# Performance work log

Hardware: AMD Instinct MI355X
Metric: run time of the kernel (lower is better)

The kernel has to match this reference:

```python
import jax, jax.numpy as jnp
import numpy as np

N = 500_000
D = 128           # input_dim
A = 128           # attention_dim
O = 1             # output_dim (broadcasts over input_dim)
B = 256           # number of repertoires (segments)


def setup_inputs() -> dict:
    key = jax.random.key(0)
    k1, k2, k3, k4 = jax.random.split(key, 4)
    x = jax.random.normal(k1, (N, D), dtype=jnp.float32)
    batch_index = jnp.sort(jax.random.randint(k2, (N,), 0, B, dtype=jnp.int32))
    # attention MLP params: Linear(D->A), Tanh, Linear(A->O)
    W1 = jax.random.normal(k3, (D, A), dtype=jnp.float32) * (1.0 / np.sqrt(D))
    b1 = jnp.zeros((A,), dtype=jnp.float32)
    W2 = jax.random.normal(k4, (A, O), dtype=jnp.float32) * (1.0 / np.sqrt(A))
    b2 = jnp.zeros((O,), dtype=jnp.float32)
    return {"x": x, "batch_index": batch_index, "W1": W1, "b1": b1, "W2": W2, "b2": b2}


def reference(x, batch_index, W1, b1, W2, b2):
    # per-instance attention score: Linear -> Tanh -> Linear
    h = jnp.tanh(x @ W1 + b1)          # [N, A]
    scores = h @ W2 + b2               # [N, O]
    # segment softmax over instances within each repertoire
    seg_max = jax.ops.segment_max(scores, batch_index, num_segments=B)   # [B, O]
    e = jnp.exp(scores - seg_max[batch_index])                           # [N, O]
    denom = jax.ops.segment_sum(e, batch_index, num_segments=B)          # [B, O]
    w = e / denom[batch_index]                                           # [N, O]
    # weighted sum of instance features per repertoire (O=1 broadcasts over D)
    out = jax.ops.segment_sum(w * x, batch_index, num_segments=B)        # [B, D]
    return out
```

## Files before the change

kernel.cpp:

```cpp
#include <hip/hip_runtime.h>
#include <math.h>

#define D_DIM 128
#define A_DIM 128
#define SPLIT 4
#define NTHREADS 256
#define TROWS 64
#define PSTRIDE 132

typedef _Float16 f16x8 __attribute__((ext_vector_type(8)));
typedef __attribute__((ext_vector_type(4))) float f32x4;

__device__ __forceinline__ float fast_tanh(float v) {
    float e = __expf(2.0f * v);
    return 1.0f - 2.0f * __builtin_amdgcn_rcpf(e + 1.0f);
}

__device__ __forceinline__ int lower_bound_i32(const int* __restrict__ arr, int n, int val) {
    int lo = 0, hi = n;
    while (lo < hi) {
        int mid = (lo + hi) >> 1;
        if (arr[mid] < val) lo = mid + 1; else hi = mid;
    }
    return lo;
}

extern "C" __global__ void __launch_bounds__(256)
seg_bounds_kernel(const int* __restrict__ bidx, int N, int B,
                  int* __restrict__ seg_start)
{
    const int i = blockIdx.x * 256 + threadIdx.x;
    if (i <= B) seg_start[i] = lower_bound_i32(bidx, N, i);
}

extern "C" __global__ void __launch_bounds__(NTHREADS)
fused_partial_kernel(const float* __restrict__ x,
                     const int* __restrict__ seg_start,
                     const float* __restrict__ W1,
                     const float* __restrict__ b1,
                     const float* __restrict__ W2,
                     float* __restrict__ part,
                     int N)
{
    __shared__ _Float16 w1s[A_DIM * D_DIM];
    __shared__ float sB1[A_DIM];
    __shared__ float sW2[A_DIM];
    __shared__ float s_lds[TROWS];
    __shared__ float o_red[16 * 32];

    const int tid = threadIdx.x;
    const int b   = blockIdx.x >> 2;
    const int q   = blockIdx.x & (SPLIT - 1);

    if (tid < A_DIM) { sB1[tid] = b1[tid]; sW2[tid] = W2[tid]; }

    for (int item = tid; item < A_DIM * 16; item += NTHREADS) {
        const int c = item & (A_DIM - 1);
        const int chunk = item >> 7;
        f16x8 vh;
        #pragma unroll
        for (int j = 0; j < 8; ++j)
            vh[j] = (_Float16)W1[(chunk * 8 + j) * A_DIM + c];
        const int addr = c * 256 + ((chunk ^ (c & 15)) << 4);
        *reinterpret_cast<f16x8*>(reinterpret_cast<char*>(w1s) + addr) = vh;
    }
    __syncthreads();

    const int lo  = seg_start[b];
    const int len = seg_start[b + 1] - lo;
    const int nt  = (len + TROWS - 1) >> 6;

    const int lane = tid & 63;
    const int wv   = tid >> 6;
    const int lc   = lane & 15;
    const int lg   = lane >> 4;

    float m = -INFINITY;
    float denom = 0.0f;
    float o_part[32];
    #pragma unroll
    for (int v = 0; v < 32; ++v) o_part[v] = 0.0f;

    float4 buf[8];
    if (q < nt) {
        const int gi = min(lo + q * TROWS + wv * 16 + lc, N - 1);
        const float4* xr = reinterpret_cast<const float4*>(x + (size_t)gi * D_DIM);
        #pragma unroll
        for (int ks = 0; ks < 4; ++ks) {
            buf[2*ks]   = xr[ks*8 + lg*2];
            buf[2*ks+1] = xr[ks*8 + lg*2 + 1];
        }
    }

    for (int tile = q; tile < nt; tile += SPLIT) {
        f16x8 ah[4], al[4];
        #pragma unroll
        for (int ks = 0; ks < 4; ++ks) {
            float vv[8] = {buf[2*ks].x, buf[2*ks].y, buf[2*ks].z, buf[2*ks].w,
                           buf[2*ks+1].x, buf[2*ks+1].y, buf[2*ks+1].z, buf[2*ks+1].w};
            #pragma unroll
            for (int j = 0; j < 8; ++j) {
                float xv = vv[j];
                _Float16 h = (_Float16)xv;
                ah[ks][j] = h;
                al[ks][j] = (_Float16)(xv - (float)h);
            }
        }

        const int next = tile + SPLIT;
        if (next < nt) {
            const int gi = min(lo + next * TROWS + wv * 16 + lc, N - 1);
            const float4* xr = reinterpret_cast<const float4*>(x + (size_t)gi * D_DIM);
            #pragma unroll
            for (int ks = 0; ks < 4; ++ks) {
                buf[2*ks]   = xr[ks*8 + lg*2];
                buf[2*ks+1] = xr[ks*8 + lg*2 + 1];
            }
        }

        float part0 = 0.f, part1 = 0.f, part2 = 0.f, part3 = 0.f;
        #pragma unroll
        for (int t = 0; t < 8; ++t) {
            f32x4 acc = {0.f, 0.f, 0.f, 0.f};
            const int c = t * 16 + lc;
            const char* base = reinterpret_cast<const char*>(w1s) + c * 256;
            #pragma unroll
            for (int ks = 0; ks < 4; ++ks) {
                const int chunk = ks * 4 + lg;
                f16x8 bh = *reinterpret_cast<const f16x8*>(
                    base + ((chunk ^ (c & 15)) << 4));
                acc = __builtin_amdgcn_mfma_f32_16x16x32_f16(ah[ks], bh, acc, 0, 0, 0);
                acc = __builtin_amdgcn_mfma_f32_16x16x32_f16(al[ks], bh, acc, 0, 0, 0);
            }
            const float b1v = sB1[c], w2v = sW2[c];
            part0 += fast_tanh(acc[0] + b1v) * w2v;
            part1 += fast_tanh(acc[1] + b1v) * w2v;
            part2 += fast_tanh(acc[2] + b1v) * w2v;
            part3 += fast_tanh(acc[3] + b1v) * w2v;
        }
        #pragma unroll
        for (int mk = 8; mk >= 1; mk >>= 1) {
            part0 += __shfl_xor(part0, mk);
            part1 += __shfl_xor(part1, mk);
            part2 += __shfl_xor(part2, mk);
            part3 += __shfl_xor(part3, mk);
        }
        if (lc == 0) {
            const int rb = wv * 16 + lg * 4;
            const int grow = tile * TROWS + rb;
            s_lds[rb + 0] = (grow + 0 < len) ? part0 : -INFINITY;
            s_lds[rb + 1] = (grow + 1 < len) ? part1 : -INFINITY;
            s_lds[rb + 2] = (grow + 2 < len) ? part2 : -INFINITY;
            s_lds[rb + 3] = (grow + 3 < len) ? part3 : -INFINITY;
        }
        __syncthreads();

        const float a0 = s_lds[lane];
        float pm = a0;
        #pragma unroll
        for (int mk = 32; mk >= 1; mk >>= 1) pm = fmaxf(pm, __shfl_xor(pm, mk));
        const float mn = fmaxf(m, pm);
        const float f  = __expf(m - mn);
        float ds = __expf(a0 - mn);
        #pragma unroll
        for (int mk = 32; mk >= 1; mk >>= 1) ds += __shfl_xor(ds, mk);
        denom = denom * f + ds;
        m = mn;

        const float w = __expf(s_lds[wv * 16 + lc] - mn);
        #pragma unroll
        for (int ks = 0; ks < 4; ++ks) {
            #pragma unroll
            for (int j = 0; j < 8; ++j) {
                const int v = ks * 8 + j;
                o_part[v] = fmaf(o_part[v], f,
                                 w * ((float)ah[ks][j] + (float)al[ks][j]));
            }
        }
        __syncthreads();
    }

    #pragma unroll
    for (int v = 0; v < 32; ++v) {
        #pragma unroll
        for (int mk = 8; mk >= 1; mk >>= 1)
            o_part[v] += __shfl_xor(o_part[v], mk);
    }
    if (lc == 0) {
        #pragma unroll
        for (int v = 0; v < 32; ++v)
            o_red[(wv * 4 + lg) * 32 + v] = o_part[v];
    }
    __syncthreads();

    float* pb = part + (size_t)blockIdx.x * PSTRIDE;
    if (tid < 128) {
        const int lg2 = tid >> 5, v = tid & 31;
        float s = 0.0f;
        #pragma unroll
        for (int w2 = 0; w2 < 4; ++w2) s += o_red[(w2 * 4 + lg2) * 32 + v];
        const int d = (v >> 3) * 32 + lg2 * 8 + (v & 7);
        pb[d] = s;
    }
    if (tid == 0) { pb[128] = m; pb[129] = denom; }
}

extern "C" __global__ void __launch_bounds__(128)
combine_kernel(const float* __restrict__ part, float* __restrict__ out)
{
    const int b = blockIdx.x, d = threadIdx.x;
    const float* pb = part + (size_t)b * SPLIT * PSTRIDE;

    float mq[SPLIT];
    float mstar = -INFINITY;
    #pragma unroll
    for (int q = 0; q < SPLIT; ++q) {
        mq[q] = pb[q * PSTRIDE + 128];
        mstar = fmaxf(mstar, mq[q]);
    }
    if (mstar == -INFINITY) {
        out[b * D_DIM + d] = 0.0f;
        return;
    }
    float den = 0.0f, val = 0.0f;
    #pragma unroll
    for (int q = 0; q < SPLIT; ++q) {
        const float e = __expf(mq[q] - mstar);
        den = fmaf(pb[q * PSTRIDE + 129], e, den);
        val = fmaf(pb[q * PSTRIDE + d],   e, val);
    }
    out[b * D_DIM + d] = val / den;
}

extern "C" void kernel_launch(void* const* d_in, const int* in_sizes, int n_in,
                              void* d_out, int out_size, void* d_ws, size_t ws_size,
                              hipStream_t stream)
{
    const float* x    = (const float*)d_in[0];
    const int*   bidx = (const int*)d_in[1];
    const float* W1   = (const float*)d_in[2];
    const float* b1   = (const float*)d_in[3];
    const float* W2   = (const float*)d_in[4];

    const int N = in_sizes[1];
    const int B = out_size / D_DIM;

    char* ws = (char*)d_ws;
    int*   seg_start = (int*)ws;
    float* part      = (float*)(ws + 4096);

    seg_bounds_kernel<<<(B + 256) / 256, 256, 0, stream>>>(bidx, N, B, seg_start);
    fused_partial_kernel<<<B * SPLIT, NTHREADS, 0, stream>>>(
        x, seg_start, W1, b1, W2, part, N);
    combine_kernel<<<B, 128, 0, stream>>>(part, (float*)d_out);
}
```

Measured before the change: 88.42 us.

## Make each wavefront run its own online softmax to drop block barriers

```diff
diff --git a/kernel.cpp b/kernel.cpp
--- a/kernel.cpp
+++ b/kernel.cpp
@@ -5,7 +5,7 @@
 #define A_DIM 128
 #define SPLIT 4
 #define NTHREADS 256
-#define TROWS 64
+#define WPS (SPLIT * 4)
 #define PSTRIDE 132
 
 typedef _Float16 f16x8 __attribute__((ext_vector_type(8)));
@@ -45,8 +45,8 @@
     __shared__ _Float16 w1s[A_DIM * D_DIM];
     __shared__ float sB1[A_DIM];
     __shared__ float sW2[A_DIM];
-    __shared__ float s_lds[TROWS];
     __shared__ float o_red[16 * 32];
+    __shared__ float s_m[4], s_d[4];
 
     const int tid = threadIdx.x;
     const int b   = blockIdx.x >> 2;
@@ -68,12 +68,13 @@
 
     const int lo  = seg_start[b];
     const int len = seg_start[b + 1] - lo;
-    const int nt  = (len + TROWS - 1) >> 6;
+    const int nt  = (len + 15) >> 4;
 
     const int lane = tid & 63;
     const int wv   = tid >> 6;
     const int lc   = lane & 15;
     const int lg   = lane >> 4;
+    const int wk   = q * 4 + wv;
 
     float m = -INFINITY;
     float denom = 0.0f;
@@ -82,8 +83,8 @@
     for (int v = 0; v < 32; ++v) o_part[v] = 0.0f;
 
     float4 buf[8];
-    if (q < nt) {
-        const int gi = min(lo + q * TROWS + wv * 16 + lc, N - 1);
+    if (wk < nt) {
+        const int gi = min(lo + wk * 16 + lc, N - 1);
         const float4* xr = reinterpret_cast<const float4*>(x + (size_t)gi * D_DIM);
         #pragma unroll
         for (int ks = 0; ks < 4; ++ks) {
@@ -92,7 +93,7 @@
         }
     }
 
-    for (int tile = q; tile < nt; tile += SPLIT) {
+    for (int tile = wk; tile < nt; tile += WPS) {
         f16x8 ah[4], al[4];
         #pragma unroll
         for (int ks = 0; ks < 4; ++ks) {
@@ -107,9 +108,9 @@
             }
         }
 
-        const int next = tile + SPLIT;
+        const int next = tile + WPS;
         if (next < nt) {
-            const int gi = min(lo + next * TROWS + wv * 16 + lc, N - 1);
+            const int gi = min(lo + next * 16 + lc, N - 1);
             const float4* xr = reinterpret_cast<const float4*>(x + (size_t)gi * D_DIM);
             #pragma unroll
             for (int ks = 0; ks < 4; ++ks) {
@@ -145,29 +146,34 @@
             part2 += __shfl_xor(part2, mk);
             part3 += __shfl_xor(part3, mk);
         }
-        if (lc == 0) {
-            const int rb = wv * 16 + lg * 4;
-            const int grow = tile * TROWS + rb;
-            s_lds[rb + 0] = (grow + 0 < len) ? part0 : -INFINITY;
-            s_lds[rb + 1] = (grow + 1 < len) ? part1 : -INFINITY;
-            s_lds[rb + 2] = (grow + 2 < len) ? part2 : -INFINITY;
-            s_lds[rb + 3] = (grow + 3 < len) ? part3 : -INFINITY;
-        }
-        __syncthreads();
-
-        const float a0 = s_lds[lane];
-        float pm = a0;
-        #pragma unroll
-        for (int mk = 32; mk >= 1; mk >>= 1) pm = fmaxf(pm, __shfl_xor(pm, mk));
+        const int rbase = tile * 16 + lg * 4;
+        const float sc0 = (rbase + 0 < len) ? part0 : -INFINITY;
+        const float sc1 = (rbase + 1 < len) ? part1 : -INFINITY;
+        const float sc2 = (rbase + 2 < len) ? part2 : -INFINITY;
+        const float sc3 = (rbase + 3 < len) ? part3 : -INFINITY;
+
+        float pm = fmaxf(fmaxf(sc0, sc1), fmaxf(sc2, sc3));
+        pm = fmaxf(pm, __shfl_xor(pm, 16));
+        pm = fmaxf(pm, __shfl_xor(pm, 32));
         const float mn = fmaxf(m, pm);
         const float f  = __expf(m - mn);
-        float ds = __expf(a0 - mn);
-        #pragma unroll
-        for (int mk = 32; mk >= 1; mk >>= 1) ds += __shfl_xor(ds, mk);
+        float ds = __expf(sc0 - mn) + __expf(sc1 - mn)
+                 + __expf(sc2 - mn) + __expf(sc3 - mn);
+        ds += __shfl_xor(ds, 16);
+        ds += __shfl_xor(ds, 32);
         denom = denom * f + ds;
         m = mn;
 
-        const float w = __expf(s_lds[wv * 16 + lc] - mn);
+        const int src = (lc >> 2) << 4;
+        const float t0 = __shfl(part0, src);
+        const float t1 = __shfl(part1, src);
+        const float t2 = __shfl(part2, src);
+        const float t3 = __shfl(part3, src);
+        const float s01 = (lc & 1) ? t1 : t0;
+        const float s23 = (lc & 1) ? t3 : t2;
+        const float my_s = (lc & 2) ? s23 : s01;
+        const float w = (tile * 16 + lc < len) ? __expf(my_s - mn) : 0.0f;
+
         #pragma unroll
         for (int ks = 0; ks < 4; ++ks) {
             #pragma unroll
@@ -177,7 +183,6 @@
                                  w * ((float)ah[ks][j] + (float)al[ks][j]));
             }
         }
-        __syncthreads();
     }
 
     #pragma unroll
@@ -191,18 +196,28 @@
         for (int v = 0; v < 32; ++v)
             o_red[(wv * 4 + lg) * 32 + v] = o_part[v];
     }
+    if (lane == 0) { s_m[wv] = m; s_d[wv] = denom; }
     __syncthreads();
 
     float* pb = part + (size_t)blockIdx.x * PSTRIDE;
     if (tid < 128) {
         const int lg2 = tid >> 5, v = tid & 31;
-        float s = 0.0f;
-        #pragma unroll
-        for (int w2 = 0; w2 < 4; ++w2) s += o_red[(w2 * 4 + lg2) * 32 + v];
+        float mstar = fmaxf(fmaxf(s_m[0], s_m[1]), fmaxf(s_m[2], s_m[3]));
+        float val = 0.0f, den = 0.0f;
+        #pragma unroll
+        for (int w2 = 0; w2 < 4; ++w2) {
+            const float mw = s_m[w2];
+            const float e  = (mw > -INFINITY) ? __expf(mw - mstar) : 0.0f;
+            val = fmaf(o_red[(w2 * 4 + lg2) * 32 + v], e, val);
+            den = fmaf(s_d[w2], e, den);
+        }
         const int d = (v >> 3) * 32 + lg2 * 8 + (v & 7);
-        pb[d] = s;
-    }
-    if (tid == 0) { pb[128] = m; pb[129] = denom; }
+        pb[d] = val;
+        if (tid == 0) { pb[128] = mstar; pb[129] = den; }
+        else if (tid == 1) {  }
+    }
+    if (tid == 64) {
+    }
 }
 
 extern "C" __global__ void __launch_bounds__(128)
@@ -225,7 +240,7 @@
     float den = 0.0f, val = 0.0f;
     #pragma unroll
     for (int q = 0; q < SPLIT; ++q) {
-        const float e = __expf(mq[q] - mstar);
+        const float e = (mq[q] > -INFINITY) ? __expf(mq[q] - mstar) : 0.0f;
         den = fmaf(pb[q * PSTRIDE + 129], e, den);
         val = fmaf(pb[q * PSTRIDE + d],   e, val);
     }
```

New measurement: 116.0 us. +31.2%, slower.
